# Kernel tuning notes

Hardware: AMD Instinct MI355X
Metric: run time of the kernel (lower is better)

Reference implementation:

```python
import jax, jax.numpy as jnp
import numpy as np

B = 2_097_152  # batch (even, pairs are (0,1),(2,3),...)
C = 25         # hardcoded: M = eye(25), logits have 25 classes
LAMDA = 0.01


def setup_inputs() -> dict:
    key = jax.random.key(0)
    k1, k2 = jax.random.split(key, 2)
    inputs = jax.random.normal(k1, (B, C), dtype=jnp.float32)
    labels = jax.random.randint(k2, (B,), 0, C)
    M = jnp.eye(C, dtype=jnp.float32)  # learned Mahalanobis matrix (init = identity, as in torch)
    return {"inputs": inputs, "labels": labels, "M": M}


def _loss(inputs, M, labels):
    # ---- metric_learning: pairs (2i, 2i+1) ----
    a, b = inputs[0::2], inputs[1::2]          # [P, C]
    la, lb = labels[0::2], labels[1::2]        # [P]
    d = jnp.abs(a - b)                         # [P, C]
    # ||M.T * d[:,None]||_F = sqrt(sum_i d[i]^2 * sum_j M[j,i]^2)
    colsq = jnp.sum(M * M, axis=0)             # [C]
    norms = jnp.sqrt((d * d) @ colsq)          # [P]

    same = la == lb                            # positive pair mask
    pos = jnp.where(same, norms, jnp.zeros_like(norms))
    distance_p = jnp.sum(pos)
    # Faithful to source bug: distance_n is OVERWRITTEN (not accumulated) on each
    # negative pair as distance_p_so_far + norm; final value comes from the LAST
    # negative pair (0 if none exist).
    excl_cum_p = jnp.cumsum(pos) - pos         # distance_p before each pair
    neg_vals = excl_cum_p + norms              # candidate distance_n per pair
    P = norms.shape[0]
    last_neg = jnp.max(jnp.where(~same, jnp.arange(P), -1))
    distance_n = jnp.where(last_neg >= 0,
                           jnp.take(neg_vals, jnp.maximum(last_neg, 0)),
                           jnp.float32(0.0))
    metric_loss = jax.nn.relu(1.0 + distance_p - distance_n)

    # ---- cross entropy (mean over batch) ----
    logp = jax.nn.log_softmax(inputs, axis=-1)                       # [B, C]
    ce = -jnp.mean(jnp.take_along_axis(logp, labels[:, None], axis=-1))

    return ce + LAMDA * metric_loss / 2.0


def reference(inputs, labels, M):
    return _loss(inputs, M, labels)
```

## Files before the change

### kernel.cpp

```cpp
#include <hip/hip_runtime.h>
#include <math.h>

namespace {

constexpr int C      = 25;
constexpr int ROWS   = 256;
constexpr int TILE_F = ROWS * C;
constexpr int NBLK   = 512;

typedef const __attribute__((address_space(1))) void* gp_t;
typedef __attribute__((address_space(3))) void* lp_t;

__device__ __forceinline__ void load16_lds(const float* g, float* l) {
  __builtin_amdgcn_global_load_lds((gp_t)g, (lp_t)l, 16, 0, 0);
}

__global__ __launch_bounds__(256)
void k_ce(const float* __restrict__ x, const int* __restrict__ labels, int B,
          double* __restrict__ ce_part, int* __restrict__ ln_part) {
  __shared__ float tile[2][TILE_F];
  __shared__ float wsum[4];
  __shared__ int   wmax[4];

  const int t      = threadIdx.x;
  const int ntiles = B / ROWS;
  const int tpb    = ntiles / NBLK;
  const int ti0    = blockIdx.x * tpb;
  const int ti1    = min(ti0 + tpb, ntiles);

  float ce_local = 0.f;
  int   best     = -1;
  int   cur      = 0;

  int lab = 0;
  if (ti0 < ti1) {
    const float* g = x + (size_t)ti0 * TILE_F;
#pragma unroll
    for (int k = 0; k < 6; ++k)
      load16_lds(g + (k * 256 + t) * 4, &tile[0][(k * 256 + t) * 4]);
    if (t < 64) load16_lds(g + (1536 + t) * 4, &tile[0][(1536 + t) * 4]);
    lab = labels[(size_t)ti0 * ROWS + t];
  }

  for (int ti = ti0; ti < ti1; ++ti) {
    __syncthreads();

    const int tnext = ti + 1;
    int labn = 0;
    if (tnext < ti1) {
      const float* g = x + (size_t)tnext * TILE_F;
      float* buf = tile[cur ^ 1];
#pragma unroll
      for (int k = 0; k < 6; ++k)
        load16_lds(g + (k * 256 + t) * 4, &buf[(k * 256 + t) * 4]);
      if (t < 64) load16_lds(g + (1536 + t) * 4, &buf[(1536 + t) * 4]);
      labn = labels[(size_t)tnext * ROWS + t];
    }

    const float* r = &tile[cur][t * C];
    float e[C];
#pragma unroll
    for (int c = 0; c < C; ++c) e[c] = r[c];

    float m = e[0];
#pragma unroll
    for (int c = 1; c < C; ++c) m = fmaxf(m, e[c]);
    float s = 0.f, xl = 0.f;
#pragma unroll
    for (int c = 0; c < C; ++c) {
      s += __expf(e[c] - m);
      xl = (c == lab) ? e[c] : xl;
    }
    ce_local += (m + __logf(s)) - xl;

    const int nxt = __shfl_down(lab, 1, 64);
    if (((t & 1) == 0) && lab != nxt) best = ((ti * ROWS) + t) >> 1;

    lab = labn;
    cur ^= 1;
  }

#pragma unroll
  for (int off = 32; off; off >>= 1) {
    ce_local += __shfl_down(ce_local, off, 64);
    best = max(best, __shfl_down(best, off, 64));
  }
  const int lane = t & 63, wid = t >> 6;
  if (lane == 0) { wsum[wid] = ce_local; wmax[wid] = best; }
  __syncthreads();
  if (t == 0) {
    ce_part[blockIdx.x] = (double)((wsum[0] + wsum[1]) + (wsum[2] + wsum[3]));
    ln_part[blockIdx.x] = max(max(wmax[0], wmax[1]), max(wmax[2], wmax[3]));
  }
}

__global__ __launch_bounds__(256)
void k_fin(const float* __restrict__ x, const float* __restrict__ M,
           const double* __restrict__ ce_part, const int* __restrict__ ln_part,
           int P, int B, float* __restrict__ out) {
  __shared__ float  colsq[C];
  __shared__ double sred[4];
  __shared__ int    ired[4];
  __shared__ double tred[4];
  __shared__ int    s_last;

  const int t = threadIdx.x, lane = t & 63, wid = t >> 6;

  if (t < C) {
    float s = 0.f;
    for (int r = 0; r < C; ++r) {
      float m = M[r * C + t];
      s += m * m;
    }
    colsq[t] = s;
  }

  double ce = 0.0;
  int ln = -1;
  for (int i = t; i < NBLK; i += 256) {
    ce += ce_part[i];
    ln = max(ln, ln_part[i]);
  }
#pragma unroll
  for (int off = 32; off; off >>= 1) {
    ce += __shfl_down(ce, off, 64);
    ln = max(ln, __shfl_down(ln, off, 64));
  }
  if (lane == 0) { sred[wid] = ce; ired[wid] = ln; }
  __syncthreads();
  if (t == 0) s_last = max(max(ired[0], ired[1]), max(ired[2], ired[3]));
  __syncthreads();
  const int last_neg = s_last;

  double tail = 0.0;
  for (int p = last_neg + 1 + t; p < P; p += 256) {
    const float* e = x + (size_t)p * (2 * C);
    float s = 0.f;
#pragma unroll
    for (int c = 0; c < C; ++c) {
      float d = e[c] - e[C + c];
      s = fmaf(d * d, colsq[c], s);
    }
    tail += (double)sqrtf(s);
  }
  float norm_last = 0.f;
  if (t == 0 && last_neg >= 0) {
    const float* e = x + (size_t)last_neg * (2 * C);
    float s = 0.f;
#pragma unroll
    for (int c = 0; c < C; ++c) {
      float d = e[c] - e[C + c];
      s = fmaf(d * d, colsq[c], s);
    }
    norm_last = sqrtf(s);
  }
#pragma unroll
  for (int off = 32; off; off >>= 1) tail += __shfl_down(tail, off, 64);
  if (lane == 0) tred[wid] = tail;
  __syncthreads();
  if (t == 0) {
    double tl    = (tred[0] + tred[1]) + (tred[2] + tred[3]);
    double cesum = (sred[0] + sred[1]) + (sred[2] + sred[3]);
    double cem   = cesum / (double)B;
    float  ml    = fmaxf(1.0f + (float)tl - norm_last, 0.0f);
    out[0] = (float)(cem + 0.005 * (double)ml);
  }
}

}

extern "C" void kernel_launch(void* const* d_in, const int* in_sizes, int n_in,
                              void* d_out, int out_size, void* d_ws,
                              size_t ws_size, hipStream_t stream) {
  const float* x      = (const float*)d_in[0];
  const int*   labels = (const int*)d_in[1];
  const float* M      = (const float*)d_in[2];
  float*       out    = (float*)d_out;

  double* ce_part = (double*)d_ws;
  int*    ln_part = (int*)((char*)d_ws + NBLK * sizeof(double));

  const int B = in_sizes[1];
  const int P = B / 2;

  k_ce<<<NBLK, 256, 0, stream>>>(x, labels, B, ce_part, ln_part);
  k_fin<<<1, 256, 0, stream>>>(x, M, ce_part, ln_part, P, B, out);
}
```

Baseline: 40.55 us.

## Triple-buffer per-wave LDS staging and drop block barriers in CE kernel

Each wavefront now stages only its own 64 rows, plus its labels, into LDS through async global_load_lds. A three-deep ring buffer lets the loop wait with s_waitcnt vmcnt instead of __syncthreads, so loads for tile ti+2 run while tile ti is computed. The aim is to hide memory latency and remove block-wide barrier stalls. The risks are more LDS per block, which lowers occupancy, and a hand-counted vmcnt that must match the number of issued loads exactly. Every wave loads 8 ops per tile (6+1+1 for lanes<16), so vmcnt(8) appears to leave one tile in flight.

```diff
diff --git a/kernel.cpp b/kernel.cpp
--- a/kernel.cpp
+++ b/kernel.cpp
@@ -6,6 +6,7 @@
 constexpr int C      = 25;
 constexpr int ROWS   = 256;
 constexpr int TILE_F = ROWS * C;
+constexpr int NBUF   = 3;
 constexpr int NBLK   = 512;
 
 typedef const __attribute__((address_space(1))) void* gp_t;
@@ -18,49 +19,41 @@
 __global__ __launch_bounds__(256)
 void k_ce(const float* __restrict__ x, const int* __restrict__ labels, int B,
           double* __restrict__ ce_part, int* __restrict__ ln_part) {
-  __shared__ float tile[2][TILE_F];
+  __shared__ float tile[NBUF][TILE_F];
+  __shared__ int   labt[NBUF][ROWS];
   __shared__ float wsum[4];
   __shared__ int   wmax[4];
 
   const int t      = threadIdx.x;
+  const int lane   = t & 63;
+  const int w      = t >> 6;
   const int ntiles = B / ROWS;
   const int tpb    = ntiles / NBLK;
   const int ti0    = blockIdx.x * tpb;
-  const int ti1    = min(ti0 + tpb, ntiles);
+  const int ti1    = ti0 + tpb;
 
   float ce_local = 0.f;
   int   best     = -1;
-  int   cur      = 0;
 
-  int lab = 0;
-  if (ti0 < ti1) {
-    const float* g = x + (size_t)ti0 * TILE_F;
+  auto stage = [&](int ti, int b) {
+    const float* gq = x + (size_t)ti * TILE_F + w * 1600;
+    float*       lq = &tile[b][w * 1600];
 #pragma unroll
     for (int k = 0; k < 6; ++k)
-      load16_lds(g + (k * 256 + t) * 4, &tile[0][(k * 256 + t) * 4]);
-    if (t < 64) load16_lds(g + (1536 + t) * 4, &tile[0][(1536 + t) * 4]);
-    lab = labels[(size_t)ti0 * ROWS + t];
-  }
+      load16_lds(gq + (k * 64 + lane) * 4, lq + (k * 64 + lane) * 4);
+    if (lane < 16) {
+      load16_lds(gq + (384 + lane) * 4, lq + (384 + lane) * 4);
+      load16_lds((const float*)(labels + (size_t)ti * ROWS + w * 64 + lane * 4),
+                 (float*)&labt[b][w * 64 + lane * 4]);
+    }
+  };
 
-  for (int ti = ti0; ti < ti1; ++ti) {
-    __syncthreads();
-
-    const int tnext = ti + 1;
-    int labn = 0;
-    if (tnext < ti1) {
-      const float* g = x + (size_t)tnext * TILE_F;
-      float* buf = tile[cur ^ 1];
-#pragma unroll
-      for (int k = 0; k < 6; ++k)
-        load16_lds(g + (k * 256 + t) * 4, &buf[(k * 256 + t) * 4]);
-      if (t < 64) load16_lds(g + (1536 + t) * 4, &buf[(1536 + t) * 4]);
-      labn = labels[(size_t)tnext * ROWS + t];
-    }
-
-    const float* r = &tile[cur][t * C];
+  auto compute = [&](int ti, int b) {
+    const float* r = &tile[b][t * C];
     float e[C];
 #pragma unroll
     for (int c = 0; c < C; ++c) e[c] = r[c];
+    const int lab = labt[b][t];
 
     float m = e[0];
 #pragma unroll
@@ -75,18 +68,27 @@
 
     const int nxt = __shfl_down(lab, 1, 64);
     if (((t & 1) == 0) && lab != nxt) best = ((ti * ROWS) + t) >> 1;
+  };
 
-    lab = labn;
-    cur ^= 1;
+  if (ti0 < ti1)     stage(ti0,     0);
+  if (ti0 + 1 < ti1) stage(ti0 + 1, 1);
+
+  int b = 0;
+  for (int ti = ti0; ti < ti1 - 1; ++ti) {
+    asm volatile("s_waitcnt vmcnt(8)" ::: "memory");
+    if (ti + 2 < ti1) stage(ti + 2, (b + 2) % NBUF);
+    compute(ti, b);
+    b = (b + 1) % NBUF;
   }
+  asm volatile("s_waitcnt vmcnt(0)" ::: "memory");
+  compute(ti1 - 1, b);
 
 #pragma unroll
   for (int off = 32; off; off >>= 1) {
     ce_local += __shfl_down(ce_local, off, 64);
     best = max(best, __shfl_down(best, off, 64));
   }
-  const int lane = t & 63, wid = t >> 6;
-  if (lane == 0) { wsum[wid] = ce_local; wmax[wid] = best; }
+  if (lane == 0) { wsum[w] = ce_local; wmax[w] = best; }
   __syncthreads();
   if (t == 0) {
     ce_part[blockIdx.x] = (double)((wsum[0] + wsum[1]) + (wsum[2] + wsum[3]));
```

After: 41.79 us. +3.1%, slower.
